# Performance work log

Hardware: AMD Instinct MI355X
Metric: run time of the kernel (lower is better)

## Reference

```python
import jax, jax.numpy as jnp
from jax import lax
import numpy as np

B, N, G, K = 4, 1024, 128, 32
D_MODEL, DEPTH, CLS = 384, 12, 40
D_INNER, D_STATE, D_CONV, DT_RANK = 768, 16, 4, 24
EPS = 1e-5
BN_SCALE = 1.0 / float(np.sqrt(1.0 + EPS))  # eval BN, running_mean=0, running_var=1


def layernorm(x, w, b):
    mu = x.mean(-1, keepdims=True)
    var = ((x - mu) ** 2).mean(-1, keepdims=True)
    return (x - mu) * lax.rsqrt(var + EPS) * w + b


def bn_eval(x, g, b):
    return x * (g * BN_SCALE) + b


def fps(xyz, n):
    Bb, Nn, _ = xyz.shape
    first = jnp.zeros((Bb,), jnp.int32)

    def step(carry, _):
        dmin, last = carry
        p = jnp.take_along_axis(xyz, last[:, None, None], axis=1)  # B,1,3
        dmin = jnp.minimum(dmin, jnp.sum((xyz - p) ** 2, -1))
        nxt = jnp.argmax(dmin, -1).astype(jnp.int32)
        return (dmin, nxt), nxt

    _, rest = lax.scan(step, (jnp.full((Bb, Nn), 1e10, xyz.dtype), first), None, length=n - 1)
    return jnp.concatenate([first[None, :], rest], 0).T  # B,G


def group_points(xyz):
    idx = fps(xyz, G)
    center = jnp.take_along_axis(xyz, idx[:, :, None], axis=1)            # B,G,3
    d2 = jnp.sum((center[:, :, None, :] - xyz[:, None, :, :]) ** 2, -1)   # B,G,N
    _, knn = lax.top_k(-d2, K)                                            # B,G,K
    nb = jax.vmap(lambda p, i: p[i])(xyz, knn)                            # B,G,K,3
    return nb - center[:, :, None, :], center


def encoder(pg, w1, b1, g1, bb1, w2, b2, w3, b3, g2, bb2, w4, b4):
    Bb, Gg, Kk, _ = pg.shape
    f = pg.reshape(Bb * Gg, Kk, 3)
    f = jax.nn.relu(bn_eval(f @ w1.T + b1, g1, bb1))                      # BG,K,128
    f = f @ w2.T + b2                                                     # BG,K,256
    fg = f.max(1, keepdims=True)
    f = jnp.concatenate([jnp.broadcast_to(fg, f.shape), f], -1)           # BG,K,512
    f = jax.nn.relu(bn_eval(f @ w3.T + b3, g2, bb2))
    f = f @ w4.T + b4
    return f.max(1).reshape(Bb, Gg, -1)                                   # B,G,C


def mamba_mixer(x, ipw, cw, cb, xpw, dpw, dpb, A_log, Dp, opw):
    L = x.shape[1]
    xz = x @ ipw.T                                                        # B,L,2*Di
    u, z = jnp.split(xz, 2, -1)
    up = jnp.pad(u, ((0, 0), (D_CONV - 1, 0), (0, 0)))                    # causal depthwise conv
    u = sum(up[:, k:k + L, :] * cw[:, k] for k in range(D_CONV)) + cb
    u = jax.nn.silu(u)
    xdb = u @ xpw.T
    dt, Bm, Cm = jnp.split(xdb, [DT_RANK, DT_RANK + D_STATE], -1)
    dt = jax.nn.softplus(dt @ dpw.T + dpb)                                # B,L,Di
    A = -jnp.exp(A_log)                                                   # Di,Ds

    def step(h, inp):
        dt_t, B_t, C_t, u_t = inp
        h = jnp.exp(dt_t[:, :, None] * A) * h + (dt_t * u_t)[:, :, None] * B_t[:, None, :]
        return h, jnp.einsum('bds,bs->bd', h, C_t)

    h0 = jnp.zeros((x.shape[0], D_INNER, D_STATE), x.dtype)
    _, ys = lax.scan(step, h0, (dt.swapaxes(0, 1), Bm.swapaxes(0, 1), Cm.swapaxes(0, 1), u.swapaxes(0, 1)))
    y = ys.swapaxes(0, 1) + u * Dp
    return (y * jax.nn.silu(z)) @ opw.T


def forward(pts, enc_w1, enc_b1, enc_bn1_g, enc_bn1_b, enc_w2, enc_b2, enc_w3, enc_b3,
            enc_bn2_g, enc_bn2_b, enc_w4, enc_b4, pos_w1, pos_b1, pos_w2, pos_b2,
            ln_w, ln_b, in_proj_w, conv_w, conv_b, x_proj_w, dt_proj_w, dt_proj_b,
            A_log, D_param, out_proj_w, normf_w, normf_b, norm_w, norm_b,
            head_w1, head_b1, head_bn1_g, head_bn1_b, head_w2, head_b2,
            head_bn2_g, head_bn2_b, head_w3, head_b3):
    nb, center = group_points(pts)
    tok = encoder(nb, enc_w1, enc_b1, enc_bn1_g, enc_bn1_b, enc_w2, enc_b2,
                  enc_w3, enc_b3, enc_bn2_g, enc_bn2_b, enc_w4, enc_b4)    # B,G,384
    pos = jax.nn.gelu(center @ pos_w1.T + pos_b1, approximate=False) @ pos_w2.T + pos_b2

    # PointMamba token reordering: sort by center x, y, z and concatenate -> L = 3G
    toks, poss = [], []
    for ax in range(3):
        o = jnp.argsort(center[:, :, ax], axis=-1)[:, :, None]
        toks.append(jnp.take_along_axis(tok, o, axis=1))
        poss.append(jnp.take_along_axis(pos, o, axis=1))
    tok = jnp.concatenate(toks, 1)
    pos = jnp.concatenate(poss, 1)

    h = tok + pos
    res = jnp.zeros_like(h)

    def layer_step(carry, p):
        h, res = carry
        lnw, lnb, ipw, cw, cb, xpw, dpw, dpb, Al, Dp, opw = p
        res = h + res
        x = layernorm(res, lnw, lnb)
        h = mamba_mixer(x, ipw, cw, cb, xpw, dpw, dpb, Al, Dp, opw)
        return (h, res), None

    (h, res), _ = lax.scan(layer_step, (h, res),
                           (ln_w, ln_b, in_proj_w, conv_w, conv_b, x_proj_w,
                            dt_proj_w, dt_proj_b, A_log, D_param, out_proj_w))
    x = layernorm(h + res, normf_w, normf_b)   # MixerModel.norm_f
    x = layernorm(x, norm_w, norm_b)           # PointMamba.norm
    feat = x.mean(1)                           # B,384
    h1 = jax.nn.relu(bn_eval(feat @ head_w1.T + head_b1, head_bn1_g, head_bn1_b))
    h2 = jax.nn.relu(bn_eval(h1 @ head_w2.T + head_b2, head_bn2_g, head_bn2_b))
    return h2 @ head_w3.T + head_b3            # B,CLS


def setup_inputs():
    key = jax.random.key(0)
    ks = iter(jax.random.split(key, 64))

    def rn(shape, s=0.02):
        return jax.random.normal(next(ks), shape, jnp.float32) * s

    inp = dict(
        pts=jax.random.normal(next(ks), (B, N, 3), jnp.float32),
        enc_w1=rn((128, 3), 0.1), enc_b1=jnp.zeros((128,)),
        enc_bn1_g=jnp.ones((128,)), enc_bn1_b=jnp.zeros((128,)),
        enc_w2=rn((256, 128), 0.05), enc_b2=jnp.zeros((256,)),
        enc_w3=rn((512, 512), 0.05), enc_b3=jnp.zeros((512,)),
        enc_bn2_g=jnp.ones((512,)), enc_bn2_b=jnp.zeros((512,)),
        enc_w4=rn((D_MODEL, 512), 0.05), enc_b4=jnp.zeros((D_MODEL,)),
        pos_w1=rn((128, 3), 0.1), pos_b1=jnp.zeros((128,)),
        pos_w2=rn((D_MODEL, 128), 0.05), pos_b2=jnp.zeros((D_MODEL,)),
        ln_w=jnp.ones((DEPTH, D_MODEL)), ln_b=jnp.zeros((DEPTH, D_MODEL)),
        in_proj_w=rn((DEPTH, 2 * D_INNER, D_MODEL)),
        conv_w=rn((DEPTH, D_INNER, D_CONV), 0.2), conv_b=jnp.zeros((DEPTH, D_INNER)),
        x_proj_w=rn((DEPTH, DT_RANK + 2 * D_STATE, D_INNER)),
        dt_proj_w=rn((DEPTH, D_INNER, DT_RANK), 0.1),
        dt_proj_b=jnp.full((DEPTH, D_INNER), -4.6, jnp.float32),
        A_log=jnp.broadcast_to(jnp.log(jnp.arange(1, D_STATE + 1, dtype=jnp.float32)),
                               (DEPTH, D_INNER, D_STATE)).copy(),
        D_param=jnp.ones((DEPTH, D_INNER)),
        out_proj_w=rn((DEPTH, D_MODEL, D_INNER)),
        normf_w=jnp.ones((D_MODEL,)), normf_b=jnp.zeros((D_MODEL,)),
        norm_w=jnp.ones((D_MODEL,)), norm_b=jnp.zeros((D_MODEL,)),
        head_w1=rn((256, D_MODEL), 0.05), head_b1=jnp.zeros((256,)),
        head_bn1_g=jnp.ones((256,)), head_bn1_b=jnp.zeros((256,)),
        head_w2=rn((256, 256), 0.05), head_b2=jnp.zeros((256,)),
        head_bn2_g=jnp.ones((256,)), head_bn2_b=jnp.zeros((256,)),
        head_w3=rn((CLS, 256), 0.05), head_b3=jnp.zeros((CLS,)),
    )
    return inp


def reference(pts, enc_w1, enc_b1, enc_bn1_g, enc_bn1_b, enc_w2, enc_b2, enc_w3, enc_b3,
              enc_bn2_g, enc_bn2_b, enc_w4, enc_b4, pos_w1, pos_b1, pos_w2, pos_b2,
              ln_w, ln_b, in_proj_w, conv_w, conv_b, x_proj_w, dt_proj_w, dt_proj_b,
              A_log, D_param, out_proj_w, normf_w, normf_b, norm_w, norm_b,
              head_w1, head_b1, head_bn1_g, head_bn1_b, head_w2, head_b2,
              head_bn2_g, head_bn2_b, head_w3, head_b3):
    return forward(pts, enc_w1, enc_b1, enc_bn1_g, enc_bn1_b, enc_w2, enc_b2, enc_w3, enc_b3,
                   enc_bn2_g, enc_bn2_b, enc_w4, enc_b4, pos_w1, pos_b1, pos_w2, pos_b2,
                   ln_w, ln_b, in_proj_w, conv_w, conv_b, x_proj_w, dt_proj_w, dt_proj_b,
                   A_log, D_param, out_proj_w, normf_w, normf_b, norm_w, norm_b,
                   head_w1, head_b1, head_bn1_g, head_bn1_b, head_w2, head_b2,
                   head_bn2_g, head_bn2_b, head_w3, head_b3)
```

## Files before the change

kernel.cpp:

```cpp
#include <hip/hip_runtime.h>
#include <hip/hip_bf16.h>

using bf16 = __hip_bfloat16;
using short8  = __attribute__((ext_vector_type(8))) short;
using floatx4 = __attribute__((ext_vector_type(4))) float;
using ull = unsigned long long;

constexpr int Bn = 4, Np = 1024, Gn = 128, Kn = 32;
constexpr int DM = 384, DEPTH = 12, CLSn = 40;
constexpr int DI = 768, DSt = 16, DTR = 24;
constexpr int Ln = 384;
constexpr int NCH = 12, CHS = 32;
constexpr int NLC = 24;
constexpr float EPSf = 1e-5f;
constexpr float BNS = 0.99999500003749968752f;
constexpr float LOG2E = 1.4426950408889634f;

static __device__ __forceinline__ short f2bf(float f){
  bf16 h = __float2bfloat16(f);
  return *reinterpret_cast<short*>(&h);
}
static __device__ __forceinline__ float fsig(float x){ return 1.f/(1.f + __expf(-x)); }
static __device__ __forceinline__ float fsoftplus(float x){
  return fmaxf(x, 0.f) + __logf(1.f + __expf(-fabsf(x)));
}

template<int CTRL>
static __device__ __forceinline__ int dppmov(int x){
  return __builtin_amdgcn_update_dpp(0, x, CTRL, 0xF, 0xF, true);
}
static __device__ __forceinline__ ull redmax64(ull key){
  #define RSTEP(CTRL) { \
    int hi = (int)(unsigned)(key >> 32), lo = (int)(unsigned)key; \
    int h2 = dppmov<CTRL>(hi), l2 = dppmov<CTRL>(lo); \
    ull k2 = ((ull)(unsigned)h2 << 32) | (unsigned)l2; \
    if (k2 > key) key = k2; }
  RSTEP(0x111) RSTEP(0x112) RSTEP(0x114) RSTEP(0x118) RSTEP(0x142) RSTEP(0x143)
  #undef RSTEP
  return key;
}

__global__ __launch_bounds__(64) void fps_kernel(const float* __restrict__ pts,
                                                 float* __restrict__ center){
  int b = blockIdx.x, t = threadIdx.x;
  __shared__ float xs[1024], ys[1024], zs[1024];
  const float* p = pts + (size_t)b * Np * 3;
  float X[16], Y[16], Z[16], D[16];
  #pragma unroll
  for (int i = 0; i < 16; ++i){
    int n = t + 64*i;
    float a = p[n*3+0], c = p[n*3+1], e = p[n*3+2];
    X[i] = a; Y[i] = c; Z[i] = e;
    xs[n] = a; ys[n] = c; zs[n] = e;
    D[i] = 1e10f;
  }
  __syncthreads();
  float px = xs[0], py = ys[0], pz = zs[0];
  if (t == 0){
    center[(size_t)(b*Gn)*3+0] = px;
    center[(size_t)(b*Gn)*3+1] = py;
    center[(size_t)(b*Gn)*3+2] = pz;
  }
  for (int it = 1; it < Gn; ++it){
    float v = -1.f; int nbest = t;
    #pragma unroll
    for (int i = 0; i < 16; ++i){
      float dx = __fsub_rn(X[i], px);
      float dy = __fsub_rn(Y[i], py);
      float dz = __fsub_rn(Z[i], pz);
      float d  = __fadd_rn(__fadd_rn(__fmul_rn(dx,dx), __fmul_rn(dy,dy)), __fmul_rn(dz,dz));
      float dm = fminf(D[i], d); D[i] = dm;
      if (dm > v){ v = dm; nbest = t + 64*i; }
    }
    ull key = ((ull)__float_as_uint(v) << 32) | (unsigned)(Np-1 - nbest);
    key = redmax64(key);
    int lo63 = __builtin_amdgcn_readlane((int)(unsigned)(key & 0xFFFFFFFFu), 63);
    int wn = Np-1 - lo63;
    wn = min(max(wn, 0), Np-1);
    px = xs[wn]; py = ys[wn]; pz = zs[wn];
    if (t == 0){
      center[(size_t)(b*Gn+it)*3+0] = px;
      center[(size_t)(b*Gn+it)*3+1] = py;
      center[(size_t)(b*Gn+it)*3+2] = pz;
    }
  }
}

__global__ __launch_bounds__(256) void knn_kernel(const float* __restrict__ pts,
                                                  const float* __restrict__ center,
                                                  float* __restrict__ nb){
  int gid = blockIdx.x; int b = gid >> 7;
  __shared__ float d2[1024];
  __shared__ float rv[4]; __shared__ int ri[4];
  int t = threadIdx.x;
  float cx = center[(size_t)gid*3+0], cy = center[(size_t)gid*3+1], cz = center[(size_t)gid*3+2];
  const float* p = pts + (size_t)b * Np * 3;
  for (int n = t; n < Np; n += 256){
    float dx = __fsub_rn(cx, p[n*3+0]);
    float dy = __fsub_rn(cy, p[n*3+1]);
    float dz = __fsub_rn(cz, p[n*3+2]);
    d2[n] = __fadd_rn(__fadd_rn(__fmul_rn(dx,dx), __fmul_rn(dy,dy)), __fmul_rn(dz,dz));
  }
  __syncthreads();
  for (int kk = 0; kk < Kn; ++kk){
    float v = 3e38f; int idx = 0;
    for (int n = t; n < Np; n += 256){
      float d = d2[n];
      if (d < v || (d == v && n < idx)){ v = d; idx = n; }
    }
    ull key = ((ull)(unsigned)(~__float_as_uint(v)) << 32) | (unsigned)(Np-1 - idx);
    key = redmax64(key);
    if ((t & 63) == 63){
      rv[t>>6] = __uint_as_float(~(unsigned)(key >> 32));
      ri[t>>6] = Np-1 - (int)(unsigned)(key & 0xFFFFFFFFu);
    }
    __syncthreads();
    if (t == 0){
      float bv = rv[0]; int bi = ri[0];
      for (int w = 1; w < 4; ++w){
        if (rv[w] < bv || (rv[w] == bv && ri[w] < bi)){ bv = rv[w]; bi = ri[w]; }
      }
      bi = min(max(bi, 0), Np-1);
      nb[((size_t)gid*Kn+kk)*3+0] = __fsub_rn(p[bi*3+0], cx);
      nb[((size_t)gid*Kn+kk)*3+1] = __fsub_rn(p[bi*3+1], cy);
      nb[((size_t)gid*Kn+kk)*3+2] = __fsub_rn(p[bi*3+2], cz);
      d2[bi] = 3e38f;
    }
    __syncthreads();
  }
}

__global__ __launch_bounds__(256) void cvt_all(const float* __restrict__ s0,
    const float* __restrict__ s1, const float* __restrict__ s2,
    const float* __restrict__ s3, const float* __restrict__ s4,
    const float* __restrict__ s5, bf16* __restrict__ dst){
  long i = ((long)blockIdx.x*256 + threadIdx.x)*4;
  if (i >= 11624448L) return;
  const float* s; long off;
  if      (i <  7077888L){ s = s0; off = 0L; }
  else if (i < 10616832L){ s = s1; off =  7077888L; }
  else if (i < 11132928L){ s = s2; off = 10616832L; }
  else if (i < 11165696L){ s = s3; off = 11132928L; }
  else if (i < 11427840L){ s = s4; off = 11165696L; }
  else                   { s = s5; off = 11427840L; }
  float4 v = *(const float4*)(s + (i - off));
  short* o = (short*)dst + i;
  o[0] = f2bf(v.x); o[1] = f2bf(v.y); o[2] = f2bf(v.z); o[3] = f2bf(v.w);
}

template<typename AT, typename WT, int ACT, int MODE>
__global__ __launch_bounds__(256) void gemm_mfma(const AT* __restrict__ A, int lda,
                                                 const WT* __restrict__ W,
                                                 const float* __restrict__ bias,
                                                 const float* __restrict__ gz,
                                                 const float* __restrict__ bbp,
                                                 float* __restrict__ C, int ldc,
                                                 int M, int N, int K){
  __shared__ __align__(16) short As[64*40];
  __shared__ __align__(16) short Ws[64*40];
  int bm = blockIdx.x * 64, bn = blockIdx.y * 64;
// ... 68 lines not shown
    if constexpr (MODE == 1){
      const float* Yr = (const float*)A + (size_t)(bm + row)*lda + k0 + kseg;
      const float* Zr = gz + (size_t)(bm + row)*1536 + 768 + k0 + kseg;
      float y[16], z[16];
      #pragma unroll
      for (int j = 0; j < 4; ++j){
        *(float4*)&y[j*4] = *(const float4*)(Yr + j*4);
        *(float4*)&z[j*4] = *(const float4*)(Zr + j*4);
      }
      short* dst = &As[row*72 + kseg];
      #pragma unroll
      for (int jj = 0; jj < 16; ++jj) dst[jj] = f2bf(y[jj] * (z[jj] * fsig(z[jj])));
    } else if constexpr (sizeof(AT) == 2){
      const short* Ar = (const short*)A + (size_t)(bm + row)*lda + k0 + kseg;
      *(short8*)&As[row*72 + kseg]     = *(const short8*)Ar;
      *(short8*)&As[row*72 + kseg + 8] = *(const short8*)(Ar + 8);
    } else {
      const float* Ar = (const float*)A + (size_t)(bm + row)*lda + k0 + kseg;
      float a[16];
      #pragma unroll
      for (int j = 0; j < 4; ++j) *(float4*)&a[j*4] = *(const float4*)(Ar + j*4);
      short* dst = &As[row*72 + kseg];
      #pragma unroll
      for (int jj = 0; jj < 16; ++jj) dst[jj] = f2bf(a[jj]);
    }
    {
      int n = bn + row;
      if constexpr (sizeof(WT) == 2){
        short8 v0, v1;
        #pragma unroll
        for (int j = 0; j < 8; ++j){ v0[j] = 0; v1[j] = 0; }
        if (n < N){
          const short* Wr = (const short*)W + (size_t)n*K + k0 + kseg;
          v0 = *(const short8*)Wr;
          v1 = *(const short8*)(Wr + 8);
        }
        *(short8*)&Ws[row*72 + kseg]     = v0;
        *(short8*)&Ws[row*72 + kseg + 8] = v1;
      } else {
        short* dst = &Ws[row*72 + kseg];
        if (n < N){
          const float* Wr = (const float*)W + (size_t)n*K + k0 + kseg;
          float wv[16];
          #pragma unroll
          for (int j = 0; j < 4; ++j) *(float4*)&wv[j*4] = *(const float4*)(Wr + j*4);
          #pragma unroll
          for (int jj = 0; jj < 16; ++jj) dst[jj] = f2bf(wv[jj]);
        } else {
          #pragma unroll
          for (int jj = 0; jj < 16; ++jj) dst[jj] = 0;
        }
      }
    }
    __syncthreads();
    short8 af0 = *(const short8*)&As[(w*16 + m16)*72 + q*8];
    short8 af1 = *(const short8*)&As[(w*16 + m16)*72 + 32 + q*8];
    #pragma unroll
    for (int j = 0; j < 4; ++j){
      short8 b0 = *(const short8*)&Ws[(j*16 + m16)*72 + q*8];
      acc[j] = __builtin_amdgcn_mfma_f32_16x16x32_bf16(af0, b0, acc[j], 0, 0, 0);
      short8 b1 = *(const short8*)&Ws[(j*16 + m16)*72 + 32 + q*8];
      acc[j] = __builtin_amdgcn_mfma_f32_16x16x32_bf16(af1, b1, acc[j], 0, 0, 0);
    }
    __syncthreads();
  }
  #pragma unroll
  for (int j = 0; j < 4; ++j){
    int n = bn + j*16 + m16;
    if (n < N){
      float bv = bias ? bias[n] : 0.f;
      float gv = 0.f, bbv = 0.f;
      if (ACT == 1){ gv = gz[n] * BNS; bbv = bbp[n]; }
      #pragma unroll
      for (int r = 0; r < 4; ++r){
        int m = bm + w*16 + q*4 + r;
        float v = acc[j][r] + bv;
        if (ACT == 1){ v = v * gv + bbv; v = fmaxf(v, 0.f); }
        C[(size_t)m*ldc + n] = v;
      }
    }
  }
}

__global__ __launch_bounds__(256) void maxk_fg(float* __restrict__ f3in){
  int gg = blockIdx.x; int c = threadIdx.x;
  float m = -3e38f;
  for (int k = 0; k < Kn; ++k) m = fmaxf(m, f3in[((size_t)gg*Kn + k)*512 + 256 + c]);
  for (int k = 0; k < Kn; ++k) f3in[((size_t)gg*Kn + k)*512 + c] = m;
}

__global__ __launch_bounds__(384) void maxk_tok(const float* __restrict__ f4, float* __restrict__ tok){
  int gg = blockIdx.x; int c = threadIdx.x;
  float m = -3e38f;
  for (int k = 0; k < Kn; ++k) m = fmaxf(m, f4[((size_t)gg*Kn + k)*DM + c]);
  tok[(size_t)gg*DM + c] = m;
}

__global__ __launch_bounds__(128) void pos_kernel(const float* __restrict__ center,
                                                  const float* __restrict__ w1, const float* __restrict__ b1,
                                                  const float* __restrict__ w2, const float* __restrict__ b2,
                                                  float* __restrict__ tok){
  int gid = blockIdx.x;
  __shared__ float h1[128]; __shared__ float c3[3];
  int t = threadIdx.x;
  if (t < 3) c3[t] = center[(size_t)gid*3 + t];
  __syncthreads();
  float a = w1[t*3+0]*c3[0] + w1[t*3+1]*c3[1] + w1[t*3+2]*c3[2] + b1[t];
  h1[t] = 0.5f * a * (1.f + erff(a * 0.70710678118654752440f));
  __syncthreads();
  for (int c = t; c < DM; c += 128){
    float s = b2[c];
    for (int j = 0; j < 128; ++j) s += w2[(size_t)c*128 + j] * h1[j];
    tok[(size_t)gid*DM + c] += s;
  }
}

__global__ __launch_bounds__(128) void sort_kernel(const float* __restrict__ center,
                                                   int* __restrict__ order){
  int bax = blockIdx.x; int b = bax / 3, ax = bax % 3;
  __shared__ float key[128];
  int t = threadIdx.x;
  key[t] = center[(size_t)(b*Gn + t)*3 + ax];
  __syncthreads();
  float kt = key[t]; int r = 0;
  for (int j = 0; j < Gn; ++j){
    float kj = key[j];
    r += (kj < kt || (kj == kt && j < t)) ? 1 : 0;
  }
  r = min(max(r, 0), Gn-1);
  order[b*Ln + ax*Gn + r] = t;
}

__global__ __launch_bounds__(256) void build_h(const float* __restrict__ tok,
                        const int* __restrict__ order,
                        float* __restrict__ h, float* __restrict__ res){
  int i = blockIdx.x * blockDim.x + threadIdx.x;
  if (i >= Bn*Ln*DM) return;
  int c = i % DM; int l = (i / DM) % Ln; int b = i / (DM*Ln);
  int src = order[b*Ln + l];
  src = min(max(src, 0), Gn-1);
  h[i] = tok[((size_t)(b*Gn + src))*DM + c];
  res[i] = 0.f;
}

__global__ __launch_bounds__(256) void ln_res_kernel(const float* __restrict__ h,
                                                     float* __restrict__ res,
                                                     bf16* __restrict__ x,
                                                     const float* __restrict__ w,
                                                     const float* __restrict__ bias){
  int wv = threadIdx.x >> 6, ln = threadIdx.x & 63;
  int tokid = blockIdx.x*4 + wv;
  const float* hr = h + (size_t)tokid*DM;
  float* rr = res + (size_t)tokid*DM;
  bf16* xr = x + (size_t)tokid*DM;
  float v[6]; float s = 0.f;
  #pragma unroll
  for (int i = 0; i < 6; ++i){ int c = ln + 64*i; float t = hr[c] + rr[c]; rr[c] = t; v[i] = t; s += t; }
  #pragma unroll
  for (int o = 32; o > 0; o >>= 1) s += __shfl_xor(s, o);
  float mu = s * (1.f/DM);
  float q = 0.f;
  #pragma unroll
  for (int i = 0; i < 6; ++i){ float d = v[i] - mu; q += d*d; }
  #pragma unroll
  for (int o = 32; o > 0; o >>= 1) q += __shfl_xor(q, o);
  float rstd = rsqrtf(q * (1.f/DM) + EPSf);
  #pragma unroll
  for (int i = 0; i < 6; ++i){ int c = ln + 64*i;
    xr[c] = __float2bfloat16((v[i]-mu)*rstd*w[c] + bias[c]); }
}

__global__ __launch_bounds__(256) void conv_fused(const float* __restrict__ xz,
                                                  float* __restrict__ ucv,
                                                  const float* __restrict__ cw,
                                                  const float* __restrict__ cb){
  int blk = blockIdx.x;
  int lc = blk % NLC; int bd = blk / NLC; int dch = bd % 3; int b = bd / 3;
  int t = threadIdx.x; int d = dch*256 + t;
  int l0 = lc*16;
  float w0 = cw[d*4+0], w1 = cw[d*4+1], w2 = cw[d*4+2], w3 = cw[d*4+3];
  float bias = cb[d];
  float u0 = (l0 >= 3) ? xz[((size_t)(b*Ln + l0-3))*1536 + d] : 0.f;
  float u1 = (l0 >= 2) ? xz[((size_t)(b*Ln + l0-2))*1536 + d] : 0.f;
  float u2 = (l0 >= 1) ? xz[((size_t)(b*Ln + l0-1))*1536 + d] : 0.f;
  const float* pin = xz + ((size_t)(b*Ln + l0))*1536 + d;
  float* pout = ucv + ((size_t)(b*Ln + l0))*DI + d;
  float r[16];
  #pragma unroll
  for (int i = 0; i < 16; ++i) r[i] = pin[(size_t)i*1536];
  #pragma unroll
  for (int i = 0; i < 16; ++i){
    float v = u0*w0 + u1*w1 + u2*w2 + r[i]*w3 + bias;
    pout[(size_t)i*DI] = v * fsig(v);
    u0 = u1; u1 = u2; u2 = r[i];
  }
}

__global__ __launch_bounds__(256) void conv_save(const float* __restrict__ xz,
                                                 float* __restrict__ bnd){
  int blk = blockIdx.x;
  int lc = blk % NLC; int bd = blk / NLC; int dch = bd % 3; int b = bd / 3;
  int t = threadIdx.x; int d = dch*256 + t;
  int l0 = lc*16;
  #pragma unroll
  for (int j = 0; j < 3; ++j){
    int l = l0 - 3 + j;
    float v = (l >= 0) ? xz[((size_t)(b*Ln + l))*1536 + d] : 0.f;
    bnd[(((size_t)blk)*3 + j)*256 + t] = v;
  }
}

__global__ __launch_bounds__(256) void conv_apply(float* __restrict__ xz,
                                                  const float* __restrict__ bnd,
                                                  const float* __restrict__ cw,
                                                  const float* __restrict__ cb){
  int blk = blockIdx.x;
  int lc = blk % NLC; int bd = blk / NLC; int dch = bd % 3; int b = bd / 3;
  int t = threadIdx.x; int d = dch*256 + t;
  int l0 = lc*16;
  float w0 = cw[d*4+0], w1 = cw[d*4+1], w2 = cw[d*4+2], w3 = cw[d*4+3];
  float bias = cb[d];
  float u0 = bnd[(((size_t)blk)*3 + 0)*256 + t];
  float u1 = bnd[(((size_t)blk)*3 + 1)*256 + t];
  float u2 = bnd[(((size_t)blk)*3 + 2)*256 + t];
  float* p = xz + ((size_t)(b*Ln + l0))*1536 + d;
  float r[16];
  #pragma unroll
  for (int i = 0; i < 16; ++i) r[i] = p[(size_t)i*1536];
  #pragma unroll
  for (int i = 0; i < 16; ++i){
    float v = u0*w0 + u1*w1 + u2*w2 + r[i]*w3 + bias;
    p[(size_t)i*1536] = v * fsig(v);
    u0 = u1; u1 = u2; u2 = r[i];
  }
}

__global__ __launch_bounds__(256) void scanA_kernel(const float* __restrict__ usrc, int uld,
                                                    const float* __restrict__ xdb,
                                                    const float* __restrict__ dpw,
                                                    const float* __restrict__ dpb,
                                                    const float* __restrict__ A_log,
                                                    float* __restrict__ SB_S,
                                                    float* __restrict__ SB_dt){
  __shared__ float sRow[CHS*56];
  __shared__ float sU[CHS*256];
  int blk = blockIdx.x;
  int c = blk % NCH; int bd = blk / NCH; int dch = bd % 3; int b = bd / 3;
  int t = threadIdx.x; int d = dch*256 + t;
  int l0 = c*CHS;
  for (int i = t; i < CHS*56; i += 256) sRow[i] = xdb[((size_t)(b*Ln + l0))*56 + i];
  const float* up = usrc + ((size_t)(b*Ln + l0))*uld + dch*256;
  #pragma unroll
  for (int i = 0; i < CHS; ++i) sU[i*256 + t] = up[(size_t)i*uld + t];
  float w[DTR];
  const float* wp = dpw + (size_t)d*DTR;
  #pragma unroll
  for (int j = 0; j < DTR; ++j) w[j] = wp[j];
  float a2[DSt], h[DSt];
  const float* ap = A_log + (size_t)d*DSt;
  #pragma unroll
  for (int s = 0; s < DSt; ++s){ a2[s] = -__expf(ap[s]) * LOG2E; h[s] = 0.f; }
  float dbias = dpb[d];
  float sumdt = 0.f;
  __syncthreads();
  for (int i = 0; i < CHS; ++i){
    int ro = i*56;
    float dtr = dbias;
    #pragma unroll
    for (int j = 0; j < DTR; ++j) dtr += w[j] * sRow[ro + j];
    float dtv = fsoftplus(dtr);
    sumdt += dtv;
    float du = dtv * sU[i*256 + t];
    #pragma unroll
    for (int s = 0; s < DSt; ++s)
      h[s] = exp2f(dtv * a2[s]) * h[s] + du * sRow[ro + 24 + s];
  }
  size_t sb = ((size_t)blk*256 + t)*16;
  #pragma unroll
  for (int s = 0; s < DSt; ++s) SB_S[sb + s] = h[s];
  SB_dt[(size_t)blk*256 + t] = sumdt;
}

__global__ __launch_bounds__(256) void scanB_kernel(float* __restrict__ ydst_base, int ys,
                                                    const float* __restrict__ usrc, int uld,
                                                    const float* __restrict__ xdb,
                                                    const float* __restrict__ dpw,
                                                    const float* __restrict__ dpb,
                                                    const float* __restrict__ A_log,
                                                    const float* __restrict__ Dp,
                                                    const float* __restrict__ SB_S,
                                                    const float* __restrict__ SB_dt){
  __shared__ float sRow[CHS*56];
  __shared__ float sU[CHS*256];
  int blk = blockIdx.x;
  int c = blk % NCH; int bd = blk / NCH; int dch = bd % 3; int b = bd / 3;
  int t = threadIdx.x; int d = dch*256 + t;
  int l0 = c*CHS;
  for (int i = t; i < CHS*56; i += 256) sRow[i] = xdb[((size_t)(b*Ln + l0))*56 + i];
  const float* up = usrc + ((size_t)(b*Ln + l0))*uld + dch*256;
  #pragma unroll
  for (int i = 0; i < CHS; ++i) sU[i*256 + t] = up[(size_t)i*uld + t];
  float w[DTR];
  const float* wp = dpw + (size_t)d*DTR;
  #pragma unroll
  for (int j = 0; j < DTR; ++j) w[j] = wp[j];
  float a2[DSt], h[DSt];
  const float* ap = A_log + (size_t)d*DSt;
  #pragma unroll
  for (int s = 0; s < DSt; ++s){ a2[s] = -__expf(ap[s]) * LOG2E; h[s] = 0.f; }
  for (int cc = 0; cc < c; ++cc){
    size_t base = (((size_t)bd*NCH + cc)*256 + t)*16;
    float sd = SB_dt[((size_t)bd*NCH + cc)*256 + t];
    #pragma unroll
    for (int s = 0; s < DSt; ++s)
      h[s] = exp2f(sd * a2[s]) * h[s] + SB_S[base + s];
  }
  float dbias = dpb[d];
  float Dd = Dp[d];
  float* ydst = ydst_base + ((size_t)(b*Ln + l0))*ys + dch*256;
  __syncthreads();
  for (int i = 0; i < CHS; ++i){
    int ro = i*56;
    float dtr = dbias;
    #pragma unroll
    for (int j = 0; j < DTR; ++j) dtr += w[j] * sRow[ro + j];
    float dtv = fsoftplus(dtr);
    float u = sU[i*256 + t];
    float du = dtv * u;
    float yv = 0.f;
    #pragma unroll
    for (int s = 0; s < DSt; ++s){
      h[s] = exp2f(dtv * a2[s]) * h[s] + du * sRow[ro + 24 + s];
      yv += h[s] * sRow[ro + 40 + s];
    }
    ydst[(size_t)i*ys + t] = yv + u*Dd;
  }
}

__global__ __launch_bounds__(256) void final_ln_kernel(const float* __restrict__ h,
                                                       const float* __restrict__ res,
                                                       const float* w1, const float* b1,
                                                       const float* w2, const float* b2,
                                                       float* __restrict__ x){
  int wv = threadIdx.x >> 6, ln = threadIdx.x & 63;
  int tokid = blockIdx.x*4 + wv;
  const float* hr = h + (size_t)tokid*DM;
  const float* rr = res + (size_t)tokid*DM;
  float* xr = x + (size_t)tokid*DM;
  float v[6]; float s = 0.f;
  #pragma unroll
  for (int i = 0; i < 6; ++i){ int c = ln + 64*i; v[i] = hr[c] + rr[c]; s += v[i]; }
  #pragma unroll
  for (int o = 32; o > 0; o >>= 1) s += __shfl_xor(s, o);
  float mu = s * (1.f/DM); float q = 0.f;
  #pragma unroll
  for (int i = 0; i < 6; ++i){ float dd = v[i]-mu; q += dd*dd; }
  #pragma unroll
  for (int o = 32; o > 0; o >>= 1) q += __shfl_xor(q, o);
  float rstd = rsqrtf(q * (1.f/DM) + EPSf);
  float u[6]; float s2 = 0.f;
  #pragma unroll
  for (int i = 0; i < 6; ++i){ int c = ln + 64*i; u[i] = (v[i]-mu)*rstd*w1[c] + b1[c]; s2 += u[i]; }
  #pragma unroll
  for (int o = 32; o > 0; o >>= 1) s2 += __shfl_xor(s2, o);
  float mu2 = s2 * (1.f/DM); float q2 = 0.f;
  #pragma unroll
  for (int i = 0; i < 6; ++i){ float dd = u[i]-mu2; q2 += dd*dd; }
  #pragma unroll
  for (int o = 32; o > 0; o >>= 1) q2 += __shfl_xor(q2, o);
  float rstd2 = rsqrtf(q2 * (1.f/DM) + EPSf);
  #pragma unroll
  for (int i = 0; i < 6; ++i){ int c = ln + 64*i; xr[c] = (u[i]-mu2)*rstd2*w2[c] + b2[c]; }
}

__global__ __launch_bounds__(384) void head_kernel(const float* __restrict__ x,
    const float* w1, const float* b1, const float* g1, const float* bb1,
    const float* w2, const float* b2, const float* g2, const float* bb2,
    const float* w3, const float* b3, float* __restrict__ out){
  int b = blockIdx.x; int t = threadIdx.x;
  __shared__ float feat[DM]; __shared__ float h1[256]; __shared__ float h2[256];
  float s = 0.f;
  for (int l = 0; l < Ln; ++l) s += x[((size_t)(b*Ln + l))*DM + t];
  feat[t] = s * (1.f/Ln);
  __syncthreads();
  if (t < 256){
    float a = b1[t];
    for (int j = 0; j < DM; ++j) a += w1[(size_t)t*DM + j] * feat[j];
    a = a * (g1[t] * BNS) + bb1[t];
    h1[t] = fmaxf(a, 0.f);
  }
  __syncthreads();
  if (t < 256){
    float a = b2[t];
    for (int j = 0; j < 256; ++j) a += w2[(size_t)t*256 + j] * h1[j];
    a = a * (g2[t] * BNS) + bb2[t];
    h2[t] = fmaxf(a, 0.f);
  }
  __syncthreads();
  if (t < CLSn){
    float a = b3[t];
    for (int j = 0; j < 256; ++j) a += w3[(size_t)t*256 + j] * h2[j];
    out[b*CLSn + t] = a;
  }
}

extern "C" void kernel_launch(void* const* d_in, const int* in_sizes, int n_in,
                              void* d_out, int out_size, void* d_ws, size_t ws_size,
                              hipStream_t stream) {
  if (n_in < 42) return;
  if (out_size < Bn*CLSn) return;
  constexpr size_t WS_FLOATS = 3919936;
  if (ws_size < WS_FLOATS * sizeof(float)) return;
  constexpr size_t MIDF = 5812224;
  constexpr size_t BIGF = 18874368;
  const bool mid = ws_size >= (WS_FLOATS + MIDF) * sizeof(float);
  const bool big = ws_size >= (WS_FLOATS + MIDF + BIGF) * sizeof(float);

  const float* pts       = (const float*)d_in[0];
  const float* enc_w1    = (const float*)d_in[1];  const float* enc_b1    = (const float*)d_in[2];
  const float* enc_bn1_g = (const float*)d_in[3];  const float* enc_bn1_b = (const float*)d_in[4];
  const float* enc_w2    = (const float*)d_in[5];  const float* enc_b2    = (const float*)d_in[6];
  const float* enc_w3    = (const float*)d_in[7];  const float* enc_b3    = (const float*)d_in[8];
  const float* enc_bn2_g = (const float*)d_in[9];  const float* enc_bn2_b = (const float*)d_in[10];
  const float* enc_w4    = (const float*)d_in[11]; const float* enc_b4    = (const float*)d_in[12];
  const float* pos_w1    = (const float*)d_in[13]; const float* pos_b1    = (const float*)d_in[14];
  const float* pos_w2    = (const float*)d_in[15]; const float* pos_b2    = (const float*)d_in[16];
  const float* ln_w      = (const float*)d_in[17]; const float* ln_b      = (const float*)d_in[18];
  const float* in_proj_w = (const float*)d_in[19];
  const float* conv_w    = (const float*)d_in[20]; const float* conv_b    = (const float*)d_in[21];
  const float* x_proj_w  = (const float*)d_in[22];
  const float* dt_proj_w = (const float*)d_in[23]; const float* dt_proj_b = (const float*)d_in[24];
  const float* A_log     = (const float*)d_in[25]; const float* D_param   = (const float*)d_in[26];
  const float* out_proj_w= (const float*)d_in[27];
  const float* normf_w   = (const float*)d_in[28]; const float* normf_b   = (const float*)d_in[29];
  const float* norm_w    = (const float*)d_in[30]; const float* norm_b    = (const float*)d_in[31];
  const float* head_w1   = (const float*)d_in[32]; const float* head_b1   = (const float*)d_in[33];
  const float* head_bn1_g= (const float*)d_in[34]; const float* head_bn1_b= (const float*)d_in[35];
  const float* head_w2   = (const float*)d_in[36]; const float* head_b2   = (const float*)d_in[37];
  const float* head_bn2_g= (const float*)d_in[38]; const float* head_bn2_b= (const float*)d_in[39];
  const float* head_w3   = (const float*)d_in[40]; const float* head_b3   = (const float*)d_in[41];

  float* ws = (float*)d_ws;
  float* hb   = ws;
  float* resb = ws + 589824;
  float* U    = ws + 1179648;
  float* center = U;
  float* nb     = U + 1536;
  float* tok    = U + 50688;
  int*   order  = (int*)(U + 247296);
  float* eb0    = U + 262144;
  float* eb1    = U + 1310720;
  float* xz   = U;
  float* xdb  = U + 2359296;
  bf16*  xb   = (bf16*)(U + 2445312);
  float* SBdt_s = U + 2445312;
  float* BND  = U + 2482176;
  float* SBS_s  = hb;
  float* xf   = U;
  float* WB = ws + WS_FLOATS;
  bf16* wb_ip = (bf16*)WB;
  bf16* wb_op = (bf16*)(WB + 3538944);
  bf16* wb_xp = (bf16*)(WB + 5308416);
  bf16* wb_e2 = (bf16*)(WB + 5566464);
  bf16* wb_e3 = (bf16*)(WB + 5582848);
  bf16* wb_e4 = (bf16*)(WB + 5713920);
  float* F3in = WB + MIDF;
  float* F3   = WB + MIDF + 8388608;
  float* F1   = WB + MIDF + 16777216;
  float* F4   = F3in;
  float* ucv  = F3in;
  float* SBS_b  = F3;
  float* SBdt_b = F1;

  if (mid)
    cvt_all<<<11352, 256, 0, stream>>>(in_proj_w, out_proj_w, x_proj_w,
                                       enc_w2, enc_w3, enc_w4, (bf16*)WB);

  fps_kernel<<<Bn, 64, 0, stream>>>(pts, center);
  knn_kernel<<<Bn*Gn, 256, 0, stream>>>(pts, center, nb);

  if (big){
    gemm_mfma<float,float,1,0><<<dim3(256,2), 256, 0, stream>>>(nb, 3, enc_w1, enc_b1,
        enc_bn1_g, enc_bn1_b, F1, 128, 16384, 128, 3);
    gemm_mfma64<float,bf16,0,0><<<dim3(256,4), 256, 0, stream>>>(F1, 128, wb_e2, enc_b2,
        nullptr, nullptr, F3in + 256, 512, 16384, 256, 128);
    maxk_fg<<<512, 256, 0, stream>>>(F3in);
    gemm_mfma64<float,bf16,1,0><<<dim3(256,8), 256, 0, stream>>>(F3in, 512, wb_e3, enc_b3,
        enc_bn2_g, enc_bn2_b, F3, 512, 16384, 512, 512);
    gemm_mfma64<float,bf16,0,0><<<dim3(256,6), 256, 0, stream>>>(F3, 512, wb_e4, enc_b4,
        nullptr, nullptr, F4, 384, 16384, 384, 512);
    maxk_tok<<<512, 384, 0, stream>>>(F4, tok);
  } else {
    for (int ch = 0; ch < 8; ++ch){
      const float* nb_c = nb + (size_t)ch*2048*3;
      float* tok_c = tok + (size_t)ch*64*DM;
      gemm_mfma<float,float,1,0><<<dim3(32,2), 256, 0, stream>>>(nb_c, 3, enc_w1, enc_b1,
          enc_bn1_g, enc_bn1_b, eb1, 128, 2048, 128, 3);
      if (mid){
        gemm_mfma64<float,bf16,0,0><<<dim3(32,4), 256, 0, stream>>>(eb1, 128, wb_e2, enc_b2,
            nullptr, nullptr, eb0 + 256, 512, 2048, 256, 128);
        maxk_fg<<<64, 256, 0, stream>>>(eb0);
        gemm_mfma64<float,bf16,1,0><<<dim3(32,8), 256, 0, stream>>>(eb0, 512, wb_e3, enc_b3,
            enc_bn2_g, enc_bn2_b, eb1, 512, 2048, 512, 512);
        gemm_mfma64<float,bf16,0,0><<<dim3(32,6), 256, 0, stream>>>(eb1, 512, wb_e4, enc_b4,
            nullptr, nullptr, eb0, 384, 2048, 384, 512);
      } else {
        gemm_mfma64<float,float,0,0><<<dim3(32,4), 256, 0, stream>>>(eb1, 128, enc_w2, enc_b2,
            nullptr, nullptr, eb0 + 256, 512, 2048, 256, 128);
        maxk_fg<<<64, 256, 0, stream>>>(eb0);
        gemm_mfma64<float,float,1,0><<<dim3(32,8), 256, 0, stream>>>(eb0, 512, enc_w3, enc_b3,
            enc_bn2_g, enc_bn2_b, eb1, 512, 2048, 512, 512);
        gemm_mfma64<float,float,0,0><<<dim3(32,6), 256, 0, stream>>>(eb1, 512, enc_w4, enc_b4,
            nullptr, nullptr, eb0, 384, 2048, 384, 512);
      }
      maxk_tok<<<64, 384, 0, stream>>>(eb0, tok_c);
    }
  }

  pos_kernel<<<Bn*Gn, 128, 0, stream>>>(center, pos_w1, pos_b1, pos_w2, pos_b2, tok);
  sort_kernel<<<Bn*3, 128, 0, stream>>>(center, order);
  build_h<<<(Bn*Ln*DM + 255)/256, 256, 0, stream>>>(tok, order, hb, resb);

  for (int l = 0; l < DEPTH; ++l){
    const float* lnw  = ln_w      + (size_t)l*DM;
    const float* lnb  = ln_b      + (size_t)l*DM;
    const float* ipw  = in_proj_w + (size_t)l*1536*DM;
    const float* cw   = conv_w    + (size_t)l*DI*4;
    const float* cb   = conv_b    + (size_t)l*DI;
    const float* xpw  = x_proj_w  + (size_t)l*56*DI;
    const float* dpw  = dt_proj_w + (size_t)l*DI*DTR;
    const float* dpb  = dt_proj_b + (size_t)l*DI;
    const float* Alg  = A_log     + (size_t)l*DI*DSt;
    const float* Dpar = D_param   + (size_t)l*DI;
    const float* opw  = out_proj_w+ (size_t)l*DM*DI;

    ln_res_kernel<<<Bn*Ln/4, 256, 0, stream>>>(hb, resb, xb, lnw, lnb);
    if (mid){
      gemm_mfma64<bf16,bf16,0,0><<<dim3(24,24), 256, 0, stream>>>(xb, DM,
          wb_ip + (size_t)l*1536*DM, nullptr, nullptr, nullptr, xz, 1536, Bn*Ln, 1536, DM);
    } else {
      gemm_mfma64<bf16,float,0,0><<<dim3(24,24), 256, 0, stream>>>(xb, DM, ipw,
          nullptr, nullptr, nullptr, xz, 1536, Bn*Ln, 1536, DM);
    }
    if (big){
      conv_fused<<<Bn*3*NLC, 256, 0, stream>>>(xz, ucv, cw, cb);
      if (mid)
        gemm_mfma64<float,bf16,0,0><<<dim3(24,1), 256, 0, stream>>>(ucv, DI,
            wb_xp + (size_t)l*56*DI, nullptr, nullptr, nullptr, xdb, 56, Bn*Ln, 56, DI);
      else
        gemm_mfma64<float,float,0,0><<<dim3(24,1), 256, 0, stream>>>(ucv, DI, xpw,
            nullptr, nullptr, nullptr, xdb, 56, Bn*Ln, 56, DI);
      scanA_kernel<<<Bn*3*NCH, 256, 0, stream>>>(ucv, DI, xdb, dpw, dpb, Alg, SBS_b, SBdt_b);
      scanB_kernel<<<Bn*3*NCH, 256, 0, stream>>>(xz, 1536, ucv, DI,
          xdb, dpw, dpb, Alg, Dpar, SBS_b, SBdt_b);
    } else {
      conv_save<<<Bn*3*NLC, 256, 0, stream>>>(xz, BND);
      conv_apply<<<Bn*3*NLC, 256, 0, stream>>>(xz, BND, cw, cb);
      if (mid)
        gemm_mfma64<float,bf16,0,0><<<dim3(24,1), 256, 0, stream>>>(xz, 1536,
            wb_xp + (size_t)l*56*DI, nullptr, nullptr, nullptr, xdb, 56, Bn*Ln, 56, DI);
      else
        gemm_mfma64<float,float,0,0><<<dim3(24,1), 256, 0, stream>>>(xz, 1536, xpw,
            nullptr, nullptr, nullptr, xdb, 56, Bn*Ln, 56, DI);
      scanA_kernel<<<Bn*3*NCH, 256, 0, stream>>>(xz, 1536, xdb, dpw, dpb, Alg, SBS_s, SBdt_s);
      scanB_kernel<<<Bn*3*NCH, 256, 0, stream>>>(xz, 1536, xz, 1536,
          xdb, dpw, dpb, Alg, Dpar, SBS_s, SBdt_s);
    }
    if (mid){
      gemm_mfma64<float,bf16,1-1,1><<<dim3(24,6), 256, 0, stream>>>(xz, 1536,
          wb_op + (size_t)l*DM*DI, nullptr, xz, nullptr, hb, DM, Bn*Ln, DM, DI);
    } else {
      gemm_mfma64<float,float,0,1><<<dim3(24,6), 256, 0, stream>>>(xz, 1536, opw,
          nullptr, xz, nullptr, hb, DM, Bn*Ln, DM, DI);
    }
  }

  final_ln_kernel<<<Bn*Ln/4, 256, 0, stream>>>(hb, resb, normf_w, normf_b, norm_w, norm_b, xf);
  head_kernel<<<Bn, 384, 0, stream>>>(xf, head_w1, head_b1, head_bn1_g, head_bn1_b,
                                      head_w2, head_b2, head_bn2_g, head_bn2_b,
                                      head_w3, head_b3, (float*)d_out);
}
```

Measured before the change: 1.598 ms.

## Fuse causal conv into x_proj GEMM and scan kernels, split-K x_proj, faster FPS argmax

Removes the separate depthwise conv kernels (conv_fused / conv_save / conv_apply) and the materialized conv output. A new xproj kernel recomputes conv+SiLU on the fly while staging the A tile, and uses split-K over the channel dimension to launch more blocks. The scan kernels recompute conv+SiLU from xz, reduce the split-K partials themselves, and save boundary rows for the in-place write. FPS replaces the 64-bit packed key reduction with two 32-bit DPP max reductions (value, then index). The cost is redundant conv recomputation in three kernels and extra partial-sum reads.

```diff
diff --git a/kernel.cpp b/kernel.cpp
--- a/kernel.cpp
+++ b/kernel.cpp
@@ -11,7 +11,7 @@
 constexpr int DI = 768, DSt = 16, DTR = 24;
 constexpr int Ln = 384;
 constexpr int NCH = 12, CHS = 32;
-constexpr int NLC = 24;
+constexpr int XDBS = 1536*56;
 constexpr float EPSf = 1e-5f;
 constexpr float BNS = 0.99999500003749968752f;
 constexpr float LOG2E = 1.4426950408889634f;
@@ -39,6 +39,12 @@
   #undef RSTEP
   return key;
 }
+static __device__ __forceinline__ int redmax32(int k){
+  #define MSTEP(CTRL) { int o = dppmov<CTRL>(k); k = max(k, o); }
+  MSTEP(0x111) MSTEP(0x112) MSTEP(0x114) MSTEP(0x118) MSTEP(0x142) MSTEP(0x143)
+  #undef MSTEP
+  return k;
+}
 
 __global__ __launch_bounds__(64) void fps_kernel(const float* __restrict__ pts,
                                                  float* __restrict__ center){
@@ -62,20 +68,35 @@
     center[(size_t)(b*Gn)*3+2] = pz;
   }
   for (int it = 1; it < Gn; ++it){
-    float v = -1.f; int nbest = t;
+    float dm[16];
     #pragma unroll
     for (int i = 0; i < 16; ++i){
       float dx = __fsub_rn(X[i], px);
       float dy = __fsub_rn(Y[i], py);
       float dz = __fsub_rn(Z[i], pz);
       float d  = __fadd_rn(__fadd_rn(__fmul_rn(dx,dx), __fmul_rn(dy,dy)), __fmul_rn(dz,dz));
-      float dm = fminf(D[i], d); D[i] = dm;
-      if (dm > v){ v = dm; nbest = t + 64*i; }
-    }
-    ull key = ((ull)__float_as_uint(v) << 32) | (unsigned)(Np-1 - nbest);
-    key = redmax64(key);
-    int lo63 = __builtin_amdgcn_readlane((int)(unsigned)(key & 0xFFFFFFFFu), 63);
-    int wn = Np-1 - lo63;
+      float v  = fminf(D[i], d); D[i] = v; dm[i] = v;
+    }
+    float m2[8], m4[4];
+    #pragma unroll
+    for (int i = 0; i < 8; ++i) m2[i] = fmaxf(dm[2*i], dm[2*i+1]);
+    #pragma unroll
+    for (int i = 0; i < 4; ++i) m4[i] = fmaxf(m2[2*i], m2[2*i+1]);
+    float vloc = fmaxf(fmaxf(m4[0], m4[1]), fmaxf(m4[2], m4[3]));
+    int kv = redmax32(__float_as_int(vloc));
+    float M = __int_as_float(__builtin_amdgcn_readlane(kv, 63));
+    int e8[8], e4[4];
+    #pragma unroll
+    for (int i = 0; i < 8; ++i){
+      int ka = (dm[2*i]   == M) ? (2047 - (t + 64*(2*i)))   : 0;
+      int kb = (dm[2*i+1] == M) ? (2047 - (t + 64*(2*i+1))) : 0;
+      e8[i] = max(ka, kb);
+    }
+    #pragma unroll
+    for (int i = 0; i < 4; ++i) e4[i] = max(e8[2*i], e8[2*i+1]);
+    int eloc = max(max(e4[0], e4[1]), max(e4[2], e4[3]));
+    eloc = redmax32(eloc);
+    int wn = 2047 - __builtin_amdgcn_readlane(eloc, 63);
     wn = min(max(wn, 0), Np-1);
     px = xs[wn]; py = ys[wn]; pz = zs[wn];
     if (t == 0){
@@ -310,6 +331,100 @@
   }
 }
 
+template<typename WT>
+__global__ __launch_bounds__(256) void xproj_kernel(const float* __restrict__ xz,
+                                                    const WT* __restrict__ W,
+                                                    const float* __restrict__ cw,
+                                                    const float* __restrict__ cb,
+                                                    float* __restrict__ xdbp,
+                                                    int KB){
+  __shared__ __align__(16) short As[64*72];
+  __shared__ __align__(16) short Ws[64*72];
+  int bm = blockIdx.x * 64;
+  int ks = blockIdx.y;
+  int t = threadIdx.x;
+  int row = t >> 2, kseg = (t & 3) * 16;
+  int w = t >> 6, lane = t & 63, m16 = lane & 15, q = lane >> 4;
+  int m = bm + row;
+  int l = m % Ln;
+  const int kbase = ks * KB;
+  floatx4 acc[4] = {};
+  const float4 z4 = make_float4(0.f, 0.f, 0.f, 0.f);
+  for (int k0 = kbase; k0 < kbase + KB; k0 += 64){
+    {
+      int ch = k0 + kseg;
+      const float* base = xz + (size_t)m*1536 + ch;
+      float x0[16], x1[16], x2[16], x3[16];
+      #pragma unroll
+      for (int j4 = 0; j4 < 4; ++j4){
+        *(float4*)&x3[j4*4] = *(const float4*)(base + j4*4);
+        *(float4*)&x2[j4*4] = (l >= 1) ? *(const float4*)(base - 1536 + j4*4) : z4;
+        *(float4*)&x1[j4*4] = (l >= 2) ? *(const float4*)(base - 2*1536 + j4*4) : z4;
+        *(float4*)&x0[j4*4] = (l >= 3) ? *(const float4*)(base - 3*1536 + j4*4) : z4;
+      }
+      short* dst = &As[row*72 + kseg];
+      #pragma unroll
+      for (int j = 0; j < 16; ++j){
+        float4 wv = *(const float4*)(cw + (size_t)(ch + j)*4);
+        float v = x0[j]*wv.x + x1[j]*wv.y + x2[j]*wv.z + x3[j]*wv.w + cb[ch + j];
+        v = v * fsig(v);
+        dst[j] = f2bf(v);
+      }
+    }
+    {
+      int n = row;
+      if constexpr (sizeof(WT) == 2){
+        short8 v0, v1;
+        #pragma unroll
+        for (int j = 0; j < 8; ++j){ v0[j] = 0; v1[j] = 0; }
+        if (n < 56){
+          const short* Wr = (const short*)W + (size_t)n*DI + k0 + kseg;
+          v0 = *(const short8*)Wr;
+          v1 = *(const short8*)(Wr + 8);
+        }
+        *(short8*)&Ws[row*72 + kseg]     = v0;
+        *(short8*)&Ws[row*72 + kseg + 8] = v1;
+      } else {
+        short* dst = &Ws[row*72 + kseg];
+        if (n < 56){
+          const float* Wr = (const float*)W + (size_t)n*DI + k0 + kseg;
+          float wv[16];
+          #pragma unroll
+          for (int j = 0; j < 4; ++j) *(float4*)&wv[j*4] = *(const float4*)(Wr + j*4);
+          #pragma unroll
+          for (int jj = 0; jj < 16; ++jj) dst[jj] = f2bf(wv[jj]);
+        } else {
+          #pragma unroll
+          for (int jj = 0; jj < 16; ++jj) dst[jj] = 0;
+        }
+      }
+    }
+    __syncthreads();
+    short8 af0 = *(const short8*)&As[(w*16 + m16)*72 + q*8];
+    short8 af1 = *(const short8*)&As[(w*16 + m16)*72 + 32 + q*8];
+    #pragma unroll
+    for (int j = 0; j < 4; ++j){
+      short8 b0 = *(const short8*)&Ws[(j*16 + m16)*72 + q*8];
+      acc[j] = __builtin_amdgcn_mfma_f32_16x16x32_bf16(af0, b0, acc[j], 0, 0, 0);
+      short8 b1 = *(const short8*)&Ws[(j*16 + m16)*72 + 32 + q*8];
+      acc[j] = __builtin_amdgcn_mfma_f32_16x16x32_bf16(af1, b1, acc[j], 0, 0, 0);
+    }
+    __syncthreads();
+  }
+  float* C = xdbp + (size_t)ks * XDBS;
+  #pragma unroll
+  for (int j = 0; j < 4; ++j){
+    int n = j*16 + m16;
+    if (n < 56){
+      #pragma unroll
+      for (int r = 0; r < 4; ++r){
+        int mm = bm + w*16 + q*4 + r;
+        C[(size_t)mm*56 + n] = acc[j][r];
+      }
+    }
+  }
+}
+
 __global__ __launch_bounds__(256) void maxk_fg(float* __restrict__ f3in){
   int gg = blockIdx.x; int c = threadIdx.x;
   float m = -3e38f;
@@ -398,88 +513,46 @@
     xr[c] = __float2bfloat16((v[i]-mu)*rstd*w[c] + bias[c]); }
 }
 
-__global__ __launch_bounds__(256) void conv_fused(const float* __restrict__ xz,
-                                                  float* __restrict__ ucv,
-                                                  const float* __restrict__ cw,
-                                                  const float* __restrict__ cb){
-  int blk = blockIdx.x;
-  int lc = blk % NLC; int bd = blk / NLC; int dch = bd % 3; int b = bd / 3;
-  int t = threadIdx.x; int d = dch*256 + t;
-  int l0 = lc*16;
-  float w0 = cw[d*4+0], w1 = cw[d*4+1], w2 = cw[d*4+2], w3 = cw[d*4+3];
-  float bias = cb[d];
-  float u0 = (l0 >= 3) ? xz[((size_t)(b*Ln + l0-3))*1536 + d] : 0.f;
-  float u1 = (l0 >= 2) ? xz[((size_t)(b*Ln + l0-2))*1536 + d] : 0.f;
-  float u2 = (l0 >= 1) ? xz[((size_t)(b*Ln + l0-1))*1536 + d] : 0.f;
-  const float* pin = xz + ((size_t)(b*Ln + l0))*1536 + d;
-  float* pout = ucv + ((size_t)(b*Ln + l0))*DI + d;
-  float r[16];
-  #pragma unroll
-  for (int i = 0; i < 16; ++i) r[i] = pin[(size_t)i*1536];
-  #pragma unroll
-  for (int i = 0; i < 16; ++i){
-    float v = u0*w0 + u1*w1 + u2*w2 + r[i]*w3 + bias;
-    pout[(size_t)i*DI] = v * fsig(v);
-    u0 = u1; u1 = u2; u2 = r[i];
-  }
-}
-
-__global__ __launch_bounds__(256) void conv_save(const float* __restrict__ xz,
-                                                 float* __restrict__ bnd){
-  int blk = blockIdx.x;
-  int lc = blk % NLC; int bd = blk / NLC; int dch = bd % 3; int b = bd / 3;
-  int t = threadIdx.x; int d = dch*256 + t;
-  int l0 = lc*16;
-  #pragma unroll
-  for (int j = 0; j < 3; ++j){
-    int l = l0 - 3 + j;
-    float v = (l >= 0) ? xz[((size_t)(b*Ln + l))*1536 + d] : 0.f;
-    bnd[(((size_t)blk)*3 + j)*256 + t] = v;
-  }
-}
-
-__global__ __launch_bounds__(256) void conv_apply(float* __restrict__ xz,
-                                                  const float* __restrict__ bnd,
-                                                  const float* __restrict__ cw,
-                                                  const float* __restrict__ cb){
-  int blk = blockIdx.x;
-  int lc = blk % NLC; int bd = blk / NLC; int dch = bd % 3; int b = bd / 3;
-  int t = threadIdx.x; int d = dch*256 + t;
-  int l0 = lc*16;
-  float w0 = cw[d*4+0], w1 = cw[d*4+1], w2 = cw[d*4+2], w3 = cw[d*4+3];
-  float bias = cb[d];
-  float u0 = bnd[(((size_t)blk)*3 + 0)*256 + t];
-  float u1 = bnd[(((size_t)blk)*3 + 1)*256 + t];
-  float u2 = bnd[(((size_t)blk)*3 + 2)*256 + t];
-  float* p = xz + ((size_t)(b*Ln + l0))*1536 + d;
-  float r[16];
-  #pragma unroll
-  for (int i = 0; i < 16; ++i) r[i] = p[(size_t)i*1536];
-  #pragma unroll
-  for (int i = 0; i < 16; ++i){
-    float v = u0*w0 + u1*w1 + u2*w2 + r[i]*w3 + bias;
-    p[(size_t)i*1536] = v * fsig(v);
-    u0 = u1; u1 = u2; u2 = r[i];
-  }
-}
-
-__global__ __launch_bounds__(256) void scanA_kernel(const float* __restrict__ usrc, int uld,
-                                                    const float* __restrict__ xdb,
+__global__ __launch_bounds__(256) void scanA_kernel(const float* __restrict__ xz,
+                                                    const float* __restrict__ xdbp, int nks,
+                                                    const float* __restrict__ cw,
+                                                    const float* __restrict__ cb,
                                                     const float* __restrict__ dpw,
                                                     const float* __restrict__ dpb,
                                                     const float* __restrict__ A_log,
                                                     float* __restrict__ SB_S,
-                                                    float* __restrict__ SB_dt){
+                                                    float* __restrict__ SB_dt,
+                                                    float* __restrict__ BND){
   __shared__ float sRow[CHS*56];
   __shared__ float sU[CHS*256];
   int blk = blockIdx.x;
   int c = blk % NCH; int bd = blk / NCH; int dch = bd % 3; int b = bd / 3;
   int t = threadIdx.x; int d = dch*256 + t;
   int l0 = c*CHS;
-  for (int i = t; i < CHS*56; i += 256) sRow[i] = xdb[((size_t)(b*Ln + l0))*56 + i];
-  const float* up = usrc + ((size_t)(b*Ln + l0))*uld + dch*256;
-  #pragma unroll
-  for (int i = 0; i < CHS; ++i) sU[i*256 + t] = up[(size_t)i*uld + t];
+  for (int i = t; i < CHS*56; i += 256){
+    size_t base = ((size_t)(b*Ln + l0))*56 + i;
+    float s = xdbp[base];
+    for (int k = 1; k < nks; ++k) s += xdbp[(size_t)k*XDBS + base];
+    sRow[i] = s;
+  }
+  float xv[CHS+3];
+  #pragma unroll
+  for (int j = 0; j < 3; ++j){
+    int ll = l0 - 3 + j;
+    xv[j] = (ll >= 0) ? xz[((size_t)(b*Ln + ll))*1536 + d] : 0.f;
+  }
+  const float* xp = xz + ((size_t)(b*Ln + l0))*1536 + d;
+  #pragma unroll
+  for (int i = 0; i < CHS; ++i) xv[3+i] = xp[(size_t)i*1536];
+  #pragma unroll
+  for (int j = 0; j < 3; ++j) BND[((size_t)blk*3 + j)*256 + t] = xv[j];
+  float cw0 = cw[d*4+0], cw1 = cw[d*4+1], cw2 = cw[d*4+2], cw3 = cw[d*4+3];
+  float cbv = cb[d];
+  #pragma unroll
+  for (int i = 0; i < CHS; ++i){
+    float v = xv[i]*cw0 + xv[i+1]*cw1 + xv[i+2]*cw2 + xv[i+3]*cw3 + cbv;
+    sU[i*256 + t] = v * fsig(v);
+  }
   float w[DTR];
   const float* wp = dpw + (size_t)d*DTR;
   #pragma unroll
@@ -509,25 +582,42 @@
   SB_dt[(size_t)blk*256 + t] = sumdt;
 }
 
-__global__ __launch_bounds__(256) void scanB_kernel(float* __restrict__ ydst_base, int ys,
-                                                    const float* __restrict__ usrc, int uld,
-                                                    const float* __restrict__ xdb,
+__global__ __launch_bounds__(256) void scanB_kernel(float* __restrict__ xz,
+                                                    const float* __restrict__ xdbp, int nks,
+                                                    const float* __restrict__ cw,
+                                                    const float* __restrict__ cb,
                                                     const float* __restrict__ dpw,
                                                     const float* __restrict__ dpb,
                                                     const float* __restrict__ A_log,
                                                     const float* __restrict__ Dp,
                                                     const float* __restrict__ SB_S,
-                                                    const float* __restrict__ SB_dt){
+                                                    const float* __restrict__ SB_dt,
+                                                    const float* __restrict__ BND){
   __shared__ float sRow[CHS*56];
   __shared__ float sU[CHS*256];
   int blk = blockIdx.x;
   int c = blk % NCH; int bd = blk / NCH; int dch = bd % 3; int b = bd / 3;
   int t = threadIdx.x; int d = dch*256 + t;
   int l0 = c*CHS;
-  for (int i = t; i < CHS*56; i += 256) sRow[i] = xdb[((size_t)(b*Ln + l0))*56 + i];
-  const float* up = usrc + ((size_t)(b*Ln + l0))*uld + dch*256;
-  #pragma unroll
-  for (int i = 0; i < CHS; ++i) sU[i*256 + t] = up[(size_t)i*uld + t];
+  for (int i = t; i < CHS*56; i += 256){
+    size_t base = ((size_t)(b*Ln + l0))*56 + i;
+    float s = xdbp[base];
+    for (int k = 1; k < nks; ++k) s += xdbp[(size_t)k*XDBS + base];
+    sRow[i] = s;
+  }
+  float xv[CHS+3];
+  #pragma unroll
+  for (int j = 0; j < 3; ++j) xv[j] = BND[((size_t)blk*3 + j)*256 + t];
+  const float* xp = xz + ((size_t)(b*Ln + l0))*1536 + d;
+  #pragma unroll
+  for (int i = 0; i < CHS; ++i) xv[3+i] = xp[(size_t)i*1536];
+  float cw0 = cw[d*4+0], cw1 = cw[d*4+1], cw2 = cw[d*4+2], cw3 = cw[d*4+3];
+  float cbv = cb[d];
+  #pragma unroll
+  for (int i = 0; i < CHS; ++i){
+    float v = xv[i]*cw0 + xv[i+1]*cw1 + xv[i+2]*cw2 + xv[i+3]*cw3 + cbv;
+    sU[i*256 + t] = v * fsig(v);
+  }
   float w[DTR];
   const float* wp = dpw + (size_t)d*DTR;
   #pragma unroll
@@ -545,7 +635,7 @@
   }
   float dbias = dpb[d];
   float Dd = Dp[d];
-  float* ydst = ydst_base + ((size_t)(b*Ln + l0))*ys + dch*256;
+  float* ydst = xz + ((size_t)(b*Ln + l0))*1536 + dch*256;
   __syncthreads();
   for (int i = 0; i < CHS; ++i){
     int ro = i*56;
@@ -561,7 +651,7 @@
       h[s] = exp2f(dtv * a2[s]) * h[s] + du * sRow[ro + 24 + s];
       yv += h[s] * sRow[ro + 40 + s];
     }
-    ydst[(size_t)i*ys + t] = yv + u*Dd;
+    ydst[(size_t)i*1536 + t] = yv + u*Dd;
   }
 }
 
@@ -696,7 +786,6 @@
   float* F3   = WB + MIDF + 8388608;
   float* F1   = WB + MIDF + 16777216;
   float* F4   = F3in;
-  float* ucv  = F3in;
   float* SBS_b  = F3;
   float* SBdt_b = F1;
 
@@ -749,6 +838,11 @@
   sort_kernel<<<Bn*3, 128, 0, stream>>>(center, order);
   build_h<<<(Bn*Ln*DM + 255)/256, 256, 0, stream>>>(tok, order, hb, resb);
 
+  const int nks = big ? 4 : 1;
+  float* xdbp = big ? F3in : xdb;
+  float* SBS  = big ? SBS_b  : SBS_s;
+  float* SBdt = big ? SBdt_b : SBdt_s;
+
   for (int l = 0; l < DEPTH; ++l){
     const float* lnw  = ln_w      + (size_t)l*DM;
     const float* lnb  = ln_b      + (size_t)l*DM;
@@ -770,30 +864,16 @@
       gemm_mfma64<bf16,float,0,0><<<dim3(24,24), 256, 0, stream>>>(xb, DM, ipw,
           nullptr, nullptr, nullptr, xz, 1536, Bn*Ln, 1536, DM);
     }
-    if (big){
-      conv_fused<<<Bn*3*NLC, 256, 0, stream>>>(xz, ucv, cw, cb);
-      if (mid)
-        gemm_mfma64<float,bf16,0,0><<<dim3(24,1), 256, 0, stream>>>(ucv, DI,
-            wb_xp + (size_t)l*56*DI, nullptr, nullptr, nullptr, xdb, 56, Bn*Ln, 56, DI);
-      else
-        gemm_mfma64<float,float,0,0><<<dim3(24,1), 256, 0, stream>>>(ucv, DI, xpw,
-            nullptr, nullptr, nullptr, xdb, 56, Bn*Ln, 56, DI);
-      scanA_kernel<<<Bn*3*NCH, 256, 0, stream>>>(ucv, DI, xdb, dpw, dpb, Alg, SBS_b, SBdt_b);
-      scanB_kernel<<<Bn*3*NCH, 256, 0, stream>>>(xz, 1536, ucv, DI,
-          xdb, dpw, dpb, Alg, Dpar, SBS_b, SBdt_b);
-    } else {
-      conv_save<<<Bn*3*NLC, 256, 0, stream>>>(xz, BND);
-      conv_apply<<<Bn*3*NLC, 256, 0, stream>>>(xz, BND, cw, cb);
-      if (mid)
-        gemm_mfma64<float,bf16,0,0><<<dim3(24,1), 256, 0, stream>>>(xz, 1536,
-            wb_xp + (size_t)l*56*DI, nullptr, nullptr, nullptr, xdb, 56, Bn*Ln, 56, DI);
-      else
-        gemm_mfma64<float,float,0,0><<<dim3(24,1), 256, 0, stream>>>(xz, 1536, xpw,
-            nullptr, nullptr, nullptr, xdb, 56, Bn*Ln, 56, DI);
-      scanA_kernel<<<Bn*3*NCH, 256, 0, stream>>>(xz, 1536, xdb, dpw, dpb, Alg, SBS_s, SBdt_s);
-      scanB_kernel<<<Bn*3*NCH, 256, 0, stream>>>(xz, 1536, xz, 1536,
-          xdb, dpw, dpb, Alg, Dpar, SBS_s, SBdt_s);
-    }
+    if (mid)
+      xproj_kernel<bf16><<<dim3(24, nks), 256, 0, stream>>>(xz,
+          wb_xp + (size_t)l*56*DI, cw, cb, xdbp, DI/nks);
+    else
+      xproj_kernel<float><<<dim3(24, nks), 256, 0, stream>>>(xz,
+          xpw, cw, cb, xdbp, DI/nks);
+    scanA_kernel<<<Bn*3*NCH, 256, 0, stream>>>(xz, xdbp, nks, cw, cb,
+        dpw, dpb, Alg, SBS, SBdt, BND);
+    scanB_kernel<<<Bn*3*NCH, 256, 0, stream>>>(xz, xdbp, nks, cw, cb,
+        dpw, dpb, Alg, Dpar, SBS, SBdt, BND);
     if (mid){
       gemm_mfma64<float,bf16,1-1,1><<<dim3(24,6), 256, 0, stream>>>(xz, 1536,
           wb_op + (size_t)l*DM*DI, nullptr, xz, nullptr, hb, DM, Bn*Ln, DM, DI);
```

Result: slower. 1.808 ms (+13.2%).
